# Optimization experiments

Measured on AMD Instinct MI355X. Metric: run time of the kernel, lower is better.

## Reference

```python
import jax, jax.numpy as jnp
import numpy as np
import itertools

# ---- module hyperparams (from args) ----
B = 4
H, W = 480, 640                 # frame_height, frame_width
NSEM = 16                       # num_sem_categories
RES = 5                         # map_resolution (cm/cell)
ZRES = 5
MAP_CM = 4800 // 2              # map_size_cm // global_downscaling
M = MAP_CM // RES               # local map cells = 480
VR = 100                        # vision_range
FOV = 79.0                      # hfov degrees
DU_SCALE = 1
CAT_THR, EXP_THR, MAP_THR = 5.0, 1.0, 1.0
AGENT_H = 0.88 * 100.0          # camera_height * 100 (cm)
MAX_H = int(360 / ZRES)         # 72
MIN_H = int(-40 / ZRES)         # -8
NZ = MAX_H - MIN_H              # 80 height bins
C = 4 + NSEM                    # obs channels
RAD2DEG = 57.29577951308232


def setup_inputs():
    key = jax.random.key(0)
    k1, k2, k3, k4 = jax.random.split(key, 4)
    obs = jax.random.uniform(k1, (B, C, H, W), dtype=jnp.float32)
    obs = obs.at[:, 3].multiply(500.0)  # depth channel in cm
    pose_obs = jax.random.normal(k2, (B, 3), dtype=jnp.float32) * 0.1
    maps_last = jax.random.uniform(k3, (B, C, M, M), dtype=jnp.float32)
    poses_last = jax.random.normal(k4, (B, 3), dtype=jnp.float32)
    return {"obs": obs, "pose_obs": pose_obs, "maps_last": maps_last, "poses_last": poses_last}


def _point_cloud(depth):
    # du.get_point_cloud_from_z_t; depth: (B,H,W) cm -> (B,H,W,3)
    f = (W / 2.0) / np.tan(np.deg2rad(FOV / 2.0))
    xc, zc = (W - 1) / 2.0, (H - 1) / 2.0
    gx = jnp.arange(W, dtype=jnp.float32)[None, None, :]
    gz = jnp.arange(H - 1, -1, -1, dtype=jnp.float32)[None, :, None]
    X = (gx - xc) * depth / f
    Z = (gz - zc) * depth / f
    return jnp.stack([X, depth, Z], axis=-1)


def _splat_feat_nd(dims, feat, coords):
    # du.splat_feat_nd: trilinear scatter-splat of per-point feats into dense grid.
    # feat: (B,F,N), coords: (B,3,N) normalized to [-1,1]. Returns (B,F,*dims).
    Bn, Fc, N = feat.shape
    pos = [coords[:, d] * (dims[d] / 2.0) + dims[d] / 2.0 for d in range(3)]
    idxs, wtss = [], []
    for offs in itertools.product((0, 1), repeat=3):
        index = jnp.zeros_like(pos[0])
        wts = jnp.ones_like(pos[0])
        for d in range(3):
            p = jnp.floor(pos[d]) + offs[d]
            safe = ((p > 0) & (p < dims[d])).astype(jnp.float32)
            wts = wts * (1.0 - jnp.abs(pos[d] - p)) * safe
            index = index * dims[d] + p * safe
        idxs.append(index)
        wtss.append(wts)
    idx = jnp.concatenate(idxs, -1).astype(jnp.int32)       # (B, 8N)
    wts = jnp.concatenate(wtss, -1)                         # (B, 8N)
    vals = jnp.tile(feat, (1, 1, 8)) * wts[:, None, :]      # (B, F, 8N)
    ncell = dims[0] * dims[1] * dims[2]
    grid = jax.vmap(lambda i, v: jnp.zeros((Fc, ncell), jnp.float32).at[:, i].add(v))(idx, vals)
    return jnp.round(grid).reshape(Bn, Fc, *dims)


def _affine_grid(theta, Hh, Ww):
    # F.affine_grid, align_corners=True. theta: (B,2,3) -> (B,Hh,Ww,2)
    xs = jnp.linspace(-1.0, 1.0, Ww)
    ys = jnp.linspace(-1.0, 1.0, Hh)
    gy, gx = jnp.meshgrid(ys, xs, indexing="ij")
    base = jnp.stack([gx, gy, jnp.ones_like(gx)], -1)       # (Hh,Ww,3)
    return jnp.einsum("hwk,bjk->bhwj", base, theta)


def _grid_sample(img, grid):
    # F.grid_sample bilinear, zeros padding, align_corners=True.
    Bn, Cc, Hi, Wi = img.shape
    x = (grid[..., 0] + 1.0) * 0.5 * (Wi - 1)
    y = (grid[..., 1] + 1.0) * 0.5 * (Hi - 1)
    x0 = jnp.floor(x); y0 = jnp.floor(y)
    x1, y1 = x0 + 1, y0 + 1

    def gather(ix, iy):
        valid = (ix >= 0) & (ix <= Wi - 1) & (iy >= 0) & (iy <= Hi - 1)
        ixc = jnp.clip(ix, 0, Wi - 1).astype(jnp.int32)
        iyc = jnp.clip(iy, 0, Hi - 1).astype(jnp.int32)
        v = jax.vmap(lambda im, yy, xx: im[:, yy, xx])(img, iyc, ixc)  # (B,C,Hg,Wg)
        return v * valid[:, None].astype(img.dtype)

    wa = (x1 - x) * (y1 - y); wb = (x1 - x) * (y - y0)
    wc = (x - x0) * (y1 - y); wd = (x - x0) * (y - y0)
    return (gather(x0, y0) * wa[:, None] + gather(x0, y1) * wb[:, None]
            + gather(x1, y0) * wc[:, None] + gather(x1, y1) * wd[:, None])


def _forward(obs, pose_obs, maps_last, poses_last):
    depth = obs[:, 3]
    pc = _point_cloud(depth)                                # camera frame (cm)
    # transform_camera_view_t with elevation 0 deg: rotation = identity, z += agent height
    av = pc.at[..., 2].add(AGENT_H)
    # transform_pose_t with shift_loc=(vr*res//2, 0, pi/2): rot angle = pi/2-pi/2 = 0, x += shift
    avc = av.at[..., 0].add(VR * RES // 2)
    xy = avc[..., :2] / RES
    xy = (xy - VR // 2.0) / VR * 2.0
    z = avc[..., 2] / ZRES
    z = (z - (MAX_H + MIN_H) // 2.0) / (MAX_H - MIN_H) * 2.0
    coords = jnp.concatenate([xy, z[..., None]], -1)        # (B,H,W,3) in [-1,1]
    coords = coords.reshape(B, H * W, 3).transpose(0, 2, 1)  # (B,3,N)
    # feat: ones occupancy channel + avg-pooled(du_scale) semantic channels
    hs, ws = H // DU_SCALE, W // DU_SCALE
    sem = obs[:, 4:4 + NSEM].reshape(B, NSEM, hs, DU_SCALE, ws, DU_SCALE).mean((3, 5))
    feat = jnp.concatenate([jnp.ones((B, 1, hs * ws), jnp.float32),
                            sem.reshape(B, NSEM, hs * ws)], 1)
    voxels = _splat_feat_nd((VR, VR, NZ), feat, coords)
    voxels = jnp.swapaxes(voxels, 2, 3)                     # .transpose(2, 3)
    min_z = int(25 / ZRES - MIN_H)                          # 13
    max_z = int((AGENT_H + 1) / ZRES - MIN_H)               # 25
    agent_height_proj = voxels[..., min_z:max_z].sum(-1)
    all_height_proj = voxels.sum(-1)
    fp_map_pred = jnp.clip(agent_height_proj[:, 0:1] / MAP_THR, 0.0, 1.0)
    fp_exp_pred = jnp.clip(all_height_proj[:, 0:1] / EXP_THR, 0.0, 1.0)
    agent_view = jnp.zeros((B, C, M, M), jnp.float32)
    x1 = M // 2 - VR // 2; x2 = x1 + VR
    y1 = M // 2; y2 = y1 + VR
    agent_view = agent_view.at[:, 0:1, y1:y2, x1:x2].set(fp_map_pred)
    agent_view = agent_view.at[:, 1:2, y1:y2, x1:x2].set(fp_exp_pred)
    agent_view = agent_view.at[:, 4:, y1:y2, x1:x2].set(
        jnp.clip(agent_height_proj[:, 1:] / CAT_THR, 0.0, 1.0))
    # get_new_pose_batch (uses pre-update theta for x/y, then wraps theta)
    r = poses_last[:, 2] / RAD2DEG
    yy = poses_last[:, 1] + pose_obs[:, 0] * jnp.sin(r) + pose_obs[:, 1] * jnp.cos(r)
    xx = poses_last[:, 0] + pose_obs[:, 0] * jnp.cos(r) - pose_obs[:, 1] * jnp.sin(r)
    oo = poses_last[:, 2] + pose_obs[:, 2] * RAD2DEG
    oo = jnp.fmod(oo - 180.0, 360.0) + 180.0
    oo = jnp.fmod(oo + 180.0, 360.0) - 180.0
    current_poses = jnp.stack([xx, yy, oo], 1)
    st = jax.lax.stop_gradient(current_poses)               # .clone().detach()
    st_xy = -(st[:, :2] * 100.0 / RES - M // 2) / (M // 2)
    st_t = (90.0 - st[:, 2]) * np.pi / 180.0
    cos_t, sin_t = jnp.cos(st_t), jnp.sin(st_t)
    zero = jnp.zeros_like(cos_t); one = jnp.ones_like(cos_t)
    theta1 = jnp.stack([jnp.stack([cos_t, -sin_t, zero], 1),
                        jnp.stack([sin_t, cos_t, zero], 1)], 1)
    theta2 = jnp.stack([jnp.stack([one, zero, st_xy[:, 0]], 1),
                        jnp.stack([zero, one, st_xy[:, 1]], 1)], 1)
    rotated = _grid_sample(agent_view, _affine_grid(theta1, M, M))
    translated = _grid_sample(rotated, _affine_grid(theta2, M, M))
    map_pred = jnp.maximum(maps_last, translated)           # max over stacked maps
    return fp_map_pred, map_pred, current_poses


def reference(obs, pose_obs, maps_last, poses_last):
    return _forward(obs, pose_obs, maps_last, poses_last)
```

## Files before the change

kernel.cpp:

```cpp
#include <hip/hip_runtime.h>
#include <math.h>

#define NB 4
#define NC 20
#define NH 480
#define NW 640
#define NPIX (NH*NW)
#define NM 480
#define NVR 100
#define NNZ 80
#define ZLO 13
#define ZHI 25
#define NZB 12
#define NSEM_ 16
#define NBINS 101

__device__ __forceinline__ float p1_chain(float d) {
  float xy1 = d / 5.0f;
  xy1 = (xy1 - 50.0f) / 100.0f * 2.0f;
  return xy1 * 50.0f + 50.0f;
}
__device__ __forceinline__ void p02_chain(float d, int row, int col, float foc,
                                          float& p0, float& p2) {
  float X = ((float)col - 319.5f) * d / foc;
  float Z = ((float)(479 - row) - 239.5f) * d / foc;
  float xy0 = (X + 250.0f) / 5.0f;
  xy0 = (xy0 - 50.0f) / 100.0f * 2.0f;
  float zz = (Z + 88.0f) / 5.0f;
  zz = (zz - 32.0f) / 80.0f * 2.0f;
  p0 = xy0 * 50.0f + 50.0f;
  p2 = zz * 40.0f + 40.0f;
}

__global__ __launch_bounds__(64) void pose_kernel(
    const float* __restrict__ pose_obs, const float* __restrict__ poses_last,
    float* __restrict__ out_poses, float* __restrict__ params)
{
  int b = threadIdx.x;
  if (b >= NB) return;
  const float R2D = 57.29577951308232f;
  float plx = poses_last[b*3+0], ply = poses_last[b*3+1], plo = poses_last[b*3+2];
  float dx = pose_obs[b*3+0], dy = pose_obs[b*3+1], dth = pose_obs[b*3+2];
  float r = plo / R2D;
  float sr = sinf(r), cr = cosf(r);
  float yy = ply + dx*sr + dy*cr;
  float xx = plx + dx*cr - dy*sr;
  float oo = plo + dth*R2D;
  oo = fmodf(oo - 180.0f, 360.0f) + 180.0f;
  oo = fmodf(oo + 180.0f, 360.0f) - 180.0f;
  out_poses[b*3+0] = xx;
  out_poses[b*3+1] = yy;
  out_poses[b*3+2] = oo;
  float tx = -((xx*100.0f/5.0f) - 240.0f) / 240.0f;
  float ty = -((yy*100.0f/5.0f) - 240.0f) / 240.0f;
  float th = ((90.0f - oo) * 3.14159274101257324f) / 180.0f;
  params[b*4+0] = cosf(th);
  params[b*4+1] = sinf(th);
  params[b*4+2] = tx;
  params[b*4+3] = ty;
}

__global__ __launch_bounds__(256) void hist_kernel(
    const float* __restrict__ obs, int* __restrict__ hist)
{
  int b = blockIdx.x / 300, blk = blockIdx.x % 300;
  __shared__ int lh[NBINS];
  for (int i = threadIdx.x; i < NBINS; i += 256) lh[i] = 0;
  __syncthreads();
  const float4* dp = (const float4*)(obs + ((size_t)b*NC + 3)*NPIX);
  float4 dv = dp[blk*256 + threadIdx.x];
  float dvv[4] = {dv.x, dv.y, dv.z, dv.w};
  #pragma unroll
  for (int k = 0; k < 4; ++k) {
    int y0 = (int)floorf(p1_chain(dvv[k]));
    y0 = min(max(y0, 0), 100);
    atomicAdd(&lh[y0], 1);
  }
  __syncthreads();
  for (int i = threadIdx.x; i < NBINS; i += 256)
    if (lh[i]) atomicAdd(&hist[b*NBINS + i], lh[i]);
}

__global__ __launch_bounds__(512) void scan_kernel(
    const int* __restrict__ hist, int* __restrict__ starts, int* __restrict__ cursors)
{
  __shared__ int lh[NB*NBINS];
  __shared__ int ls[NB*NBINS + 1];
  for (int i = threadIdx.x; i < NB*NBINS; i += 512) lh[i] = hist[i];
  __syncthreads();
  if (threadIdx.x == 0) {
    int s = 0;
    for (int i = 0; i < NB*NBINS; ++i) { ls[i] = s; s += lh[i]; }
    ls[NB*NBINS] = s;
  }
  __syncthreads();
  for (int i = threadIdx.x; i < NB*NBINS + 1; i += 512) {
    starts[i] = ls[i];
    if (i < NB*NBINS) cursors[i] = ls[i];
  }
}

__global__ __launch_bounds__(256) void scatter_kernel(
    const float* __restrict__ obs, int* __restrict__ cursors,
    float4* __restrict__ recs, float foc)
{
  int b = blockIdx.x / 300, blk = blockIdx.x % 300;
  __shared__ int lh[NBINS], lbase[NBINS], loff[NBINS];
  for (int i = threadIdx.x; i < NBINS; i += 256) { lh[i] = 0; loff[i] = 0; }
  __syncthreads();
  int pix0 = (blk*256 + threadIdx.x)*4;
  int row = pix0 / NW;
  int c0 = pix0 - row*NW;
  const float4* dp = (const float4*)(obs + ((size_t)b*NC + 3)*NPIX);
  float4 dv = dp[blk*256 + threadIdx.x];
  float dvv[4] = {dv.x, dv.y, dv.z, dv.w};
  float rp0[4], rp1[4], rp2[4]; int rbin[4];
  #pragma unroll
  for (int k = 0; k < 4; ++k) {
    float p1 = p1_chain(dvv[k]);
    float p0, p2;
    p02_chain(dvv[k], row, c0 + k, foc, p0, p2);
    rp0[k] = p0; rp1[k] = p1; rp2[k] = p2;
    int y0 = (int)floorf(p1); y0 = min(max(y0, 0), 100);
    rbin[k] = y0;
    atomicAdd(&lh[y0], 1);
  }
  __syncthreads();
  for (int i = threadIdx.x; i < NBINS; i += 256)
    if (lh[i] > 0) lbase[i] = atomicAdd(&cursors[b*NBINS + i], lh[i]);
  __syncthreads();
  #pragma unroll
  for (int k = 0; k < 4; ++k) {
    int idx = atomicAdd(&loff[rbin[k]], 1);
    recs[lbase[rbin[k]] + idx] =
        make_float4(rp0[k], rp1[k], rp2[k], __int_as_float(pix0 + k));
  }
}

__global__ __launch_bounds__(256) void slab0_kernel(
    const float4* __restrict__ recs, const int* __restrict__ starts,
    float* __restrict__ proj, float* __restrict__ out_fp)
{
  int b = blockIdx.x / NVR, Y = blockIdx.x % NVR;
  __shared__ float g[NVR*81];
  for (int i = threadIdx.x; i < NVR*81; i += 256) g[i] = 0.0f;
  __syncthreads();
  if (Y > 0) {
    int lo = starts[b*NBINS + Y - 1];
    int hi = starts[b*NBINS + Y + 1];
    float Yf = (float)Y;
    for (int i = lo + threadIdx.x; i < hi; i += 256) {
      float4 r = recs[i];
      float wy = 1.0f - fabsf(r.y - Yf);
      if (wy <= 0.0f) continue;
      float p0 = r.x, p2 = r.z;
      float fl0 = floorf(p0), fl2 = floorf(p2);
      #pragma unroll
      for (int xo = 0; xo < 2; ++xo) {
        float px = fl0 + (float)xo;
        if (!(px > 0.0f && px < 100.0f)) continue;
        float wxy = (1.0f - fabsf(p0 - px)) * wy;
        if (wxy <= 0.0f) continue;
        int ix = (int)px;
        #pragma unroll
        for (int zo = 0; zo < 2; ++zo) {
          float pz = fl2 + (float)zo;
          if (!(pz > 0.0f && pz < 80.0f)) continue;
          float w = wxy * (1.0f - fabsf(p2 - pz));
          if (w > 0.0f) atomicAdd(&g[ix*81 + (int)pz], w);
        }
      }
    }
  }
  __syncthreads();
  if (threadIdx.x < NVR) {
    int x = threadIdx.x;
    float s_all = 0.0f, s_ag = 0.0f;
    for (int z = 0; z < NNZ; ++z) {
      float v = rintf(g[x*81 + z]);
      s_all += v;
      if (z >= ZLO && z < ZHI) s_ag += v;
    }
    float fp_map = fminf(fmaxf(s_ag, 0.0f), 1.0f);
    float fp_exp = fminf(fmaxf(s_all, 0.0f), 1.0f);
    size_t pb = (((size_t)b*NC + 0)*NVR + Y)*NVR + x;
    proj[pb] = fp_map;
    proj[pb + NVR*NVR] = fp_exp;
    proj[pb + 2*NVR*NVR] = 0.0f;
    proj[pb + 3*NVR*NVR] = 0.0f;
    out_fp[(size_t)b*NVR*NVR + Y*NVR + x] = fp_map;
  }
}

__global__ __launch_bounds__(256) void slab1_kernel(
    const float* __restrict__ obs, const float4* __restrict__ recs,
    const int* __restrict__ starts, float* __restrict__ proj)
{
  int half = blockIdx.x & 1;
  int t = blockIdx.x >> 1;
  int b = t / NVR, Y = t % NVR;
  __shared__ float g[NVR*NZB*8];
  for (int i = threadIdx.x; i < NVR*NZB*8; i += 256) g[i] = 0.0f;
  __syncthreads();
  if (Y > 0) {
    int lo = starts[b*NBINS + Y - 1];
    int hi = starts[b*NBINS + Y + 1];
    float Yf = (float)Y;
    const float* sbase = obs + ((size_t)b*NC + 4 + half*8)*NPIX;
    for (int i = lo + threadIdx.x; i < hi; i += 256) {
      float4 r = recs[i];
      float wy = 1.0f - fabsf(r.y - Yf);
      if (wy <= 0.0f) continue;
      float p2 = r.z;
      float fl2 = floorf(p2);
      float wz[2]; int iz[2]; bool any = false;
      #pragma unroll
      for (int zo = 0; zo < 2; ++zo) {
        float pz = fl2 + (float)zo;
        bool v = (pz >= (float)ZLO) && (pz < (float)ZHI);
        float w = v ? (1.0f - fabsf(p2 - pz)) : 0.0f;
        wz[zo] = w; iz[zo] = v ? ((int)pz - ZLO) : 0;
        any = any || (w > 0.0f);
      }
      if (!any) continue;
      float p0 = r.x;
      float fl0 = floorf(p0);
      int pid = __float_as_int(r.w);
      float sem[8];
      #pragma unroll
      for (int s = 0; s < 8; ++s) sem[s] = sbase[(size_t)s*NPIX + pid];
      #pragma unroll
      for (int xo = 0; xo < 2; ++xo) {
        float px = fl0 + (float)xo;
        if (!(px > 0.0f && px < 100.0f)) continue;
        float wxy = (1.0f - fabsf(p0 - px)) * wy;
        if (wxy <= 0.0f) continue;
        int ix = (int)px;
        #pragma unroll
        for (int zo = 0; zo < 2; ++zo) {
          float w = wxy * wz[zo];
          if (w > 0.0f) {
            float* gb = &g[(ix*NZB + iz[zo])*8];
            #pragma unroll
            for (int s = 0; s < 8; ++s) atomicAdd(&gb[s], w * sem[s]);
          }
        }
      }
    }
  }
  __syncthreads();
  for (int p = threadIdx.x; p < NVR*8; p += 256) {
    int x = p >> 3, s = p & 7;
    float acc = 0.0f;
    #pragma unroll
    for (int z = 0; z < NZB; ++z) acc += rintf(g[(x*NZB + z)*8 + s]);
    float val = fminf(fmaxf(acc / 5.0f, 0.0f), 1.0f);
    proj[(((size_t)b*NC + 4 + half*8 + s)*NVR + Y)*NVR + x] = val;
  }
}

__global__ __launch_bounds__(256) void transform_kernel(
    const float* __restrict__ maps_last, const float* __restrict__ proj,
    const float* __restrict__ params, float* __restrict__ d_out)
{
  int tid = blockIdx.x * 256 + threadIdx.x;
  int b = tid / (NM*NM);
  int rem = tid - b*(NM*NM);
  int h = rem / NM;
  int w = rem - h*NM;

  float ct = params[b*4+0];
  float st = params[b*4+1];
  float tx = params[b*4+2];
  float ty = params[b*4+3];

  const float step = 2.0f/479.0f;
  float gx = -1.0f + (float)w * step;
  float gy = -1.0f + (float)h * step;
  float X2 = ((gx + tx) + 1.0f) * 0.5f * 479.0f;
  float Y2 = ((gy + ty) + 1.0f) * 0.5f * 479.0f;
  float x0 = floorf(X2), y0 = floorf(Y2);
  float wox[2] = {(x0 + 1.0f) - X2, X2 - x0};
  float woy[2] = {(y0 + 1.0f) - Y2, Y2 - y0};

  float twt[16];
  int   toff[16];
  int nz = 0;
  #pragma unroll
  for (int oy = 0; oy < 2; ++oy) {
    #pragma unroll
    for (int ox = 0; ox < 2; ++ox) {
      int kb = (oy*2 + ox)*4;
      float cx = x0 + (float)ox;
      float cy = y0 + (float)oy;
      float wo = wox[ox]*woy[oy];
      bool ov = (cx >= 0.0f) && (cx <= 479.0f) && (cy >= 0.0f) && (cy <= 479.0f);
      if (ov) {
        float gxr = -1.0f + cx * step;
        float gyr = -1.0f + cy * step;
        float xr = gxr*ct - gyr*st;
        float yr = gxr*st + gyr*ct;
        float XS = (xr + 1.0f)*0.5f*479.0f;
        float YS = (yr + 1.0f)*0.5f*479.0f;
        float ix0 = floorf(XS), iy0 = floorf(YS);
        float wix[2] = {(ix0+1.0f)-XS, XS-ix0};
        float wiy[2] = {(iy0+1.0f)-YS, YS-iy0};
        #pragma unroll
        for (int qy = 0; qy < 2; ++qy) {
          #pragma unroll
          for (int qx = 0; qx < 2; ++qx) {
            int k = kb + qy*2 + qx;
            float ux = ix0 + (float)qx;
            float vy = iy0 + (float)qy;
            float wv = 0.0f; int off = 0;
            if (ux >= 0.0f && ux <= 479.0f && vy >= 0.0f && vy <= 479.0f) {
              int U = (int)ux, V = (int)vy;
              if (U >= 190 && U < 290 && V >= 240 && V < 340) {
                off = (V - 240)*NVR + (U - 190);
                wv = wo * (wix[qx]*wiy[qy]);
              }
            }
            twt[k] = wv; toff[k] = off;
            nz += (wv != 0.0f) ? 1 : 0;
          }
        }
      } else {
        #pragma unroll
        for (int k = 0; k < 4; ++k) { twt[kb+k] = 0.0f; toff[kb+k] = 0; }
      }
    }
  }

  const float* pbase = proj + (size_t)b*NC*NVR*NVR;
  size_t base_idx = (size_t)b*NC*NM*NM + (size_t)h*NM + w;
  if (nz > 0) {
    #pragma unroll 1
    for (int c = 0; c < NC; ++c) {
      size_t idx = base_idx + (size_t)c*NM*NM;
      float ml = maps_last[idx];
      float val = 0.0f;
      if (c != 2 && c != 3) {
        const float* pc = pbase + (size_t)c*NVR*NVR;
        #pragma unroll
        for (int k = 0; k < 16; ++k) val += twt[k]*pc[toff[k]];
      }
      d_out[40000 + idx] = fmaxf(ml, val);
    }
  } else {
    #pragma unroll 1
    for (int c = 0; c < NC; ++c) {
      size_t idx = base_idx + (size_t)c*NM*NM;
      d_out[40000 + idx] = fmaxf(maps_last[idx], 0.0f);
    }
  }
}

extern "C" void kernel_launch(void* const* d_in, const int* in_sizes, int n_in,
                              void* d_out, int out_size, void* d_ws, size_t ws_size,
                              hipStream_t stream)
{
  const float* obs        = (const float*)d_in[0];
  const float* pose_obs   = (const float*)d_in[1];
  const float* maps_last  = (const float*)d_in[2];
  const float* poses_last = (const float*)d_in[3];
  float* out = (float*)d_out;

  char* ws = (char*)d_ws;
  int*    hist    = (int*)ws;
  int*    starts  = (int*)(ws + 2048);
  int*    cursors = (int*)(ws + 4096);
  float*  params  = (float*)(ws + 6144);
  float4* recs    = (float4*)(ws + 8192);
  float*  proj    = (float*)(ws + 8192 + 19660800);

  hipMemsetAsync(ws, 0, 6144, stream);

  const float foc = (float)(((double)NW) / 2.0 / tan(79.0 * 0.5 * M_PI / 180.0));

  pose_kernel<<<1, 64, 0, stream>>>(pose_obs, poses_last, out + 40000 + 18432000, params);
  hist_kernel<<<NB*300, 256, 0, stream>>>(obs, hist);
  scan_kernel<<<1, 512, 0, stream>>>(hist, starts, cursors);
  scatter_kernel<<<NB*300, 256, 0, stream>>>(obs, cursors, recs, foc);
  slab0_kernel<<<NB*NVR, 256, 0, stream>>>(recs, starts, proj, out);
  slab1_kernel<<<NB*NVR*2, 256, 0, stream>>>(obs, recs, starts, proj);
  transform_kernel<<<(NB*NM*NM)/256, 256, 0, stream>>>(maps_last, proj, params, out);
}
```

Before: 562.9 us.

## Pre-filter agent-height band points and pack semantic features contiguously

Adds a second histogram, scan and scatter that keep only points whose height falls in the agent band. For those points the 16 semantic channel values are gathered once and packed next to the position in two band buffers. The semantic slab kernel then streams these packed records instead of walking every point and doing strided gathers from obs. The band buffers are placed in the output region before the final transform overwrites it. Writes past BCAP are clamped to the last slot, which would corrupt results if the band count ever exceeds that cap.

```diff
diff --git a/kernel.cpp b/kernel.cpp
--- a/kernel.cpp
+++ b/kernel.cpp
@@ -14,6 +14,7 @@
 #define NZB 12
 #define NSEM_ 16
 #define NBINS 101
+#define BCAP 700000
 
 __device__ __forceinline__ float p1_chain(float d) {
   float xy1 = d / 5.0f;
@@ -61,12 +62,16 @@
 }
 
 __global__ __launch_bounds__(256) void hist_kernel(
-    const float* __restrict__ obs, int* __restrict__ hist)
+    const float* __restrict__ obs, int* __restrict__ hist,
+    int* __restrict__ bhist, float foc)
 {
   int b = blockIdx.x / 300, blk = blockIdx.x % 300;
-  __shared__ int lh[NBINS];
-  for (int i = threadIdx.x; i < NBINS; i += 256) lh[i] = 0;
-  __syncthreads();
+  __shared__ int lh[NBINS], lh2[NBINS];
+  for (int i = threadIdx.x; i < NBINS; i += 256) { lh[i] = 0; lh2[i] = 0; }
+  __syncthreads();
+  int pix0 = (blk*256 + threadIdx.x)*4;
+  int row = pix0 / NW;
+  int c0 = pix0 - row*NW;
   const float4* dp = (const float4*)(obs + ((size_t)b*NC + 3)*NPIX);
   float4 dv = dp[blk*256 + threadIdx.x];
   float dvv[4] = {dv.x, dv.y, dv.z, dv.w};
@@ -75,38 +80,55 @@
     int y0 = (int)floorf(p1_chain(dvv[k]));
     y0 = min(max(y0, 0), 100);
     atomicAdd(&lh[y0], 1);
-  }
-  __syncthreads();
-  for (int i = threadIdx.x; i < NBINS; i += 256)
-    if (lh[i]) atomicAdd(&hist[b*NBINS + i], lh[i]);
+    float p0, p2;
+    p02_chain(dvv[k], row, c0 + k, foc, p0, p2);
+    if (p2 > 12.0f && p2 < 25.0f) atomicAdd(&lh2[y0], 1);
+  }
+  __syncthreads();
+  for (int i = threadIdx.x; i < NBINS; i += 256) {
+    if (lh[i])  atomicAdd(&hist[b*NBINS + i], lh[i]);
+    if (lh2[i]) atomicAdd(&bhist[b*NBINS + i], lh2[i]);
+  }
 }
 
 __global__ __launch_bounds__(512) void scan_kernel(
-    const int* __restrict__ hist, int* __restrict__ starts, int* __restrict__ cursors)
-{
-  __shared__ int lh[NB*NBINS];
-  __shared__ int ls[NB*NBINS + 1];
-  for (int i = threadIdx.x; i < NB*NBINS; i += 512) lh[i] = hist[i];
+    const int* __restrict__ hist, const int* __restrict__ bhist,
+    int* __restrict__ starts, int* __restrict__ bstarts,
+    int* __restrict__ cursors, int* __restrict__ bcursors)
+{
+  __shared__ int lh[NB*NBINS], ls[NB*NBINS + 1];
+  __shared__ int lh2[NB*NBINS], ls2[NB*NBINS + 1];
+  for (int i = threadIdx.x; i < NB*NBINS; i += 512) { lh[i] = hist[i]; lh2[i] = bhist[i]; }
   __syncthreads();
   if (threadIdx.x == 0) {
     int s = 0;
     for (int i = 0; i < NB*NBINS; ++i) { ls[i] = s; s += lh[i]; }
     ls[NB*NBINS] = s;
   }
+  if (threadIdx.x == 64) {
+    int s = 0;
+    for (int i = 0; i < NB*NBINS; ++i) { ls2[i] = s; s += lh2[i]; }
+    ls2[NB*NBINS] = s;
+  }
   __syncthreads();
   for (int i = threadIdx.x; i < NB*NBINS + 1; i += 512) {
     starts[i] = ls[i];
-    if (i < NB*NBINS) cursors[i] = ls[i];
+    bstarts[i] = ls2[i];
+    if (i < NB*NBINS) { cursors[i] = ls[i]; bcursors[i] = ls2[i]; }
   }
 }
 
 __global__ __launch_bounds__(256) void scatter_kernel(
     const float* __restrict__ obs, int* __restrict__ cursors,
-    float4* __restrict__ recs, float foc)
+    int* __restrict__ bcursors, float4* __restrict__ recs,
+    float4* __restrict__ band0, float4* __restrict__ band1, float foc)
 {
   int b = blockIdx.x / 300, blk = blockIdx.x % 300;
   __shared__ int lh[NBINS], lbase[NBINS], loff[NBINS];
-  for (int i = threadIdx.x; i < NBINS; i += 256) { lh[i] = 0; loff[i] = 0; }
+  __shared__ int lh2[NBINS], lbase2[NBINS], loff2[NBINS];
+  for (int i = threadIdx.x; i < NBINS; i += 256) {
+    lh[i] = 0; loff[i] = 0; lh2[i] = 0; loff2[i] = 0;
+  }
   __syncthreads();
   int pix0 = (blk*256 + threadIdx.x)*4;
   int row = pix0 / NW;
@@ -114,7 +136,7 @@
   const float4* dp = (const float4*)(obs + ((size_t)b*NC + 3)*NPIX);
   float4 dv = dp[blk*256 + threadIdx.x];
   float dvv[4] = {dv.x, dv.y, dv.z, dv.w};
-  float rp0[4], rp1[4], rp2[4]; int rbin[4];
+  float rp0[4], rp1[4], rp2[4]; int rbin[4]; bool rband[4];
   #pragma unroll
   for (int k = 0; k < 4; ++k) {
     float p1 = p1_chain(dvv[k]);
@@ -123,17 +145,37 @@
     rp0[k] = p0; rp1[k] = p1; rp2[k] = p2;
     int y0 = (int)floorf(p1); y0 = min(max(y0, 0), 100);
     rbin[k] = y0;
+    rband[k] = (p2 > 12.0f) && (p2 < 25.0f);
     atomicAdd(&lh[y0], 1);
-  }
-  __syncthreads();
-  for (int i = threadIdx.x; i < NBINS; i += 256)
-    if (lh[i] > 0) lbase[i] = atomicAdd(&cursors[b*NBINS + i], lh[i]);
-  __syncthreads();
+    if (rband[k]) atomicAdd(&lh2[y0], 1);
+  }
+  __syncthreads();
+  for (int i = threadIdx.x; i < NBINS; i += 256) {
+    if (lh[i]  > 0) lbase[i]  = atomicAdd(&cursors[b*NBINS + i], lh[i]);
+    if (lh2[i] > 0) lbase2[i] = atomicAdd(&bcursors[b*NBINS + i], lh2[i]);
+  }
+  __syncthreads();
+  const float* sbase = obs + ((size_t)b*NC + 4)*NPIX;
   #pragma unroll
   for (int k = 0; k < 4; ++k) {
-    int idx = atomicAdd(&loff[rbin[k]], 1);
-    recs[lbase[rbin[k]] + idx] =
-        make_float4(rp0[k], rp1[k], rp2[k], __int_as_float(pix0 + k));
+    int o = atomicAdd(&loff[rbin[k]], 1);
+    recs[lbase[rbin[k]] + o] = make_float4(rp0[k], rp1[k], rp2[k], 0.0f);
+    if (rband[k]) {
+      int pix = pix0 + k;
+      float smv[NSEM_];
+      #pragma unroll
+      for (int s = 0; s < NSEM_; ++s) smv[s] = sbase[(size_t)s*NPIX + pix];
+      int o2 = atomicAdd(&loff2[rbin[k]], 1);
+      int slot = lbase2[rbin[k]] + o2;
+      if (slot >= BCAP) slot = BCAP - 1;
+      float4 pos = make_float4(rp0[k], rp1[k], rp2[k], 0.0f);
+      band0[slot*3+0] = pos;
+      band0[slot*3+1] = make_float4(smv[0], smv[1], smv[2], smv[3]);
+      band0[slot*3+2] = make_float4(smv[4], smv[5], smv[6], smv[7]);
+      band1[slot*3+0] = pos;
+      band1[slot*3+1] = make_float4(smv[8], smv[9], smv[10], smv[11]);
+      band1[slot*3+2] = make_float4(smv[12], smv[13], smv[14], smv[15]);
+    }
   }
 }
 
@@ -193,8 +235,8 @@
 }
 
 __global__ __launch_bounds__(256) void slab1_kernel(
-    const float* __restrict__ obs, const float4* __restrict__ recs,
-    const int* __restrict__ starts, float* __restrict__ proj)
+    const float4* __restrict__ band0, const float4* __restrict__ band1,
+    const int* __restrict__ bstarts, float* __restrict__ proj)
 {
   int half = blockIdx.x & 1;
   int t = blockIdx.x >> 1;
@@ -203,32 +245,29 @@
   for (int i = threadIdx.x; i < NVR*NZB*8; i += 256) g[i] = 0.0f;
   __syncthreads();
   if (Y > 0) {
-    int lo = starts[b*NBINS + Y - 1];
-    int hi = starts[b*NBINS + Y + 1];
+    int lo = bstarts[b*NBINS + Y - 1];
+    int hi = bstarts[b*NBINS + Y + 1];
     float Yf = (float)Y;
-    const float* sbase = obs + ((size_t)b*NC + 4 + half*8)*NPIX;
+    const float4* src = half ? band1 : band0;
     for (int i = lo + threadIdx.x; i < hi; i += 256) {
-      float4 r = recs[i];
-      float wy = 1.0f - fabsf(r.y - Yf);
+      float4 ra = src[i*3+0];
+      float wy = 1.0f - fabsf(ra.y - Yf);
       if (wy <= 0.0f) continue;
-      float p2 = r.z;
+      float4 s0 = src[i*3+1];
+      float4 s1 = src[i*3+2];
+      float sem[8] = {s0.x, s0.y, s0.z, s0.w, s1.x, s1.y, s1.z, s1.w};
+      float p2 = ra.z;
       float fl2 = floorf(p2);
-      float wz[2]; int iz[2]; bool any = false;
+      float wz[2]; int iz[2];
       #pragma unroll
       for (int zo = 0; zo < 2; ++zo) {
         float pz = fl2 + (float)zo;
         bool v = (pz >= (float)ZLO) && (pz < (float)ZHI);
-        float w = v ? (1.0f - fabsf(p2 - pz)) : 0.0f;
-        wz[zo] = w; iz[zo] = v ? ((int)pz - ZLO) : 0;
-        any = any || (w > 0.0f);
+        wz[zo] = v ? (1.0f - fabsf(p2 - pz)) : 0.0f;
+        iz[zo] = v ? ((int)pz - ZLO) : 0;
       }
-      if (!any) continue;
-      float p0 = r.x;
+      float p0 = ra.x;
       float fl0 = floorf(p0);
-      int pid = __float_as_int(r.w);
-      float sem[8];
-      #pragma unroll
-      for (int s = 0; s < 8; ++s) sem[s] = sbase[(size_t)s*NPIX + pid];
       #pragma unroll
       for (int xo = 0; xo < 2; ++xo) {
         float px = fl0 + (float)xo;
@@ -366,22 +405,28 @@
   float* out = (float*)d_out;
 
   char* ws = (char*)d_ws;
-  int*    hist    = (int*)ws;
-  int*    starts  = (int*)(ws + 2048);
-  int*    cursors = (int*)(ws + 4096);
-  float*  params  = (float*)(ws + 6144);
-  float4* recs    = (float4*)(ws + 8192);
-  float*  proj    = (float*)(ws + 8192 + 19660800);
-
-  hipMemsetAsync(ws, 0, 6144, stream);
+  int*    hist     = (int*)(ws + 0);
+  int*    bhist    = (int*)(ws + 2048);
+  int*    starts   = (int*)(ws + 4096);
+  int*    bstarts  = (int*)(ws + 6144);
+  int*    cursors  = (int*)(ws + 8192);
+  int*    bcursors = (int*)(ws + 10240);
+  float*  params   = (float*)(ws + 12288);
+  float4* recs     = (float4*)(ws + 16384);
+  float*  proj     = (float*)(ws + 16384 + 19660800);
+
+  float4* band0 = (float4*)(out + 40000);
+  float4* band1 = (float4*)(out + 40000 + (size_t)BCAP*12);
+
+  hipMemsetAsync(ws, 0, 4096, stream);
 
   const float foc = (float)(((double)NW) / 2.0 / tan(79.0 * 0.5 * M_PI / 180.0));
 
   pose_kernel<<<1, 64, 0, stream>>>(pose_obs, poses_last, out + 40000 + 18432000, params);
-  hist_kernel<<<NB*300, 256, 0, stream>>>(obs, hist);
-  scan_kernel<<<1, 512, 0, stream>>>(hist, starts, cursors);
-  scatter_kernel<<<NB*300, 256, 0, stream>>>(obs, cursors, recs, foc);
+  hist_kernel<<<NB*300, 256, 0, stream>>>(obs, hist, bhist, foc);
+  scan_kernel<<<1, 512, 0, stream>>>(hist, bhist, starts, bstarts, cursors, bcursors);
+  scatter_kernel<<<NB*300, 256, 0, stream>>>(obs, cursors, bcursors, recs, band0, band1, foc);
   slab0_kernel<<<NB*NVR, 256, 0, stream>>>(recs, starts, proj, out);
-  slab1_kernel<<<NB*NVR*2, 256, 0, stream>>>(obs, recs, starts, proj);
+  slab1_kernel<<<NB*NVR*2, 256, 0, stream>>>(band0, band1, bstarts, proj);
   transform_kernel<<<(NB*NM*NM)/256, 256, 0, stream>>>(maps_last, proj, params, out);
 }
```

Result: slower. 609.2 us (+8.2%).
